# Performance work log

Hardware: AMD Instinct MI355X
Metric: run time of the kernel (lower is better)

Reference implementation:

```python
import jax, jax.numpy as jnp
import numpy as np
from jax import lax

B, S, K, H, NCLS = 64, 2048, 2, 256, 2
D = K * K  # input_dim = conv_kernel ** 2


def setup_inputs() -> dict:
    key = jax.random.key(0)
    ks = jax.random.split(key, 12)
    s = 0.1
    return {
        "x": jax.random.normal(ks[0], (B, S, D), dtype=jnp.float32),
        # elementwise quanvolution-style conv filter (k x k)
        "conv_w": jax.random.normal(ks[1], (K, K), dtype=jnp.float32) * s,
        "conv_b": jax.random.normal(ks[2], (K, K), dtype=jnp.float32) * s,
        # LSTM params, torch gate order (i, f, g, o)
        "w_ih": jax.random.normal(ks[3], (4 * H, D), dtype=jnp.float32) * s,
        "w_hh": jax.random.normal(ks[4], (4 * H, H), dtype=jnp.float32) * s,
        "b_ih": jax.random.normal(ks[5], (4 * H,), dtype=jnp.float32) * s,
        "b_hh": jax.random.normal(ks[6], (4 * H,), dtype=jnp.float32) * s,
        # classifier: depth=2 ReLU layers + final Linear(H, NCLS)
        "w1": jax.random.normal(ks[7], (H, H), dtype=jnp.float32) * s,
        "b1": jnp.zeros((H,), dtype=jnp.float32),
        "w2": jax.random.normal(ks[8], (H, H), dtype=jnp.float32) * s,
        "b2": jnp.zeros((H,), dtype=jnp.float32),
        "w3": jax.random.normal(ks[9], (NCLS, H), dtype=jnp.float32) * s,
        "b3": jnp.zeros((NCLS,), dtype=jnp.float32),
    }


def _lstm(feat, w_ih, w_hh, b_ih, b_hh):
    # feat: [B, S, D] -> hidden states [B, S, H]
    b, _, _ = feat.shape
    h_dim = w_hh.shape[1]
    bias = b_ih + b_hh
    # precompute input projections for all timesteps (batched GEMM)
    gates_x = jnp.einsum('bsd,gd->bsg', feat, w_ih) + bias  # [B, S, 4H]

    def step(carry, gx):
        h, c = carry
        gates = gx + h @ w_hh.T  # [B, 4H]
        i, f, g, o = jnp.split(gates, 4, axis=-1)
        i, f, o = jax.nn.sigmoid(i), jax.nn.sigmoid(f), jax.nn.sigmoid(o)
        g = jnp.tanh(g)
        c = f * c + i * g
        h = o * jnp.tanh(c)
        return (h, c), h

    init = (jnp.zeros((b, h_dim), feat.dtype), jnp.zeros((b, h_dim), feat.dtype))
    _, hs = lax.scan(step, init, gates_x.transpose(1, 0, 2))  # hs: [S, B, H]
    return hs.transpose(1, 0, 2)


def reference(x, conv_w, conv_b, w_ih, w_hh, b_ih, b_hh, w1, b1, w2, b2, w3, b3):
    b, s, _ = x.shape
    # batched replacement of the per-patch CPU conv loop
    patches = x.reshape(b, s, K, K)
    feat = jax.nn.sigmoid(patches * conv_w + conv_b).reshape(b, s, K * K)
    lstm_out = _lstm(feat, w_ih, w_hh, b_ih, b_hh)  # [B, S, H]
    h1 = jax.nn.relu(lstm_out @ w1.T + b1)
    h2 = jax.nn.relu(h1 @ w2.T + b2)
    logits = h2 @ w3.T + b3  # [B, S, NCLS]
    return logits
```

## Files before the change

kernel.cpp:

```cpp
#include <hip/hip_runtime.h>


#define BB 64
#define SS 2048
#define HH 256

typedef _Float16 f16;
typedef _Float16 h2 __attribute__((ext_vector_type(2)));
typedef _Float16 v8h __attribute__((ext_vector_type(8)));

union V8H { v8h v; h2 p[4]; };

__device__ __forceinline__ float fdot2f(h2 a, h2 b, float c){
#if __has_builtin(__builtin_amdgcn_fdot2)
  return __builtin_amdgcn_fdot2(a, b, c, false);
#else
  return c + (float)a.x*(float)b.x + (float)a.y*(float)b.y;
#endif
}

__device__ __forceinline__ float psum2(float x){
#if __has_builtin(__builtin_amdgcn_mov_dpp)
  x += __int_as_float(__builtin_amdgcn_mov_dpp(__float_as_int(x), 0xB1, 0xf, 0xf, true));
#else
  x += __shfl_xor(x, 1, 64);
#endif
  return x;
}

__device__ __forceinline__ float rcpf_(float x){
#if __has_builtin(__builtin_amdgcn_rcpf)
  return __builtin_amdgcn_rcpf(x);
#else
  return 1.f/x;
#endif
}
__device__ __forceinline__ float sigmf_(float x){ return rcpf_(1.f + __expf(-x)); }
__device__ __forceinline__ float tanhf_(float x){
  x = fminf(fmaxf(x, -15.f), 15.f);
  float e = __expf(2.f*x);
  return (e - 1.f)*rcpf_(e + 1.f);
}
__device__ __forceinline__ h2 mkh2(float a, float b){ h2 r; r.x=(f16)a; r.y=(f16)b; return r; }

__device__ __forceinline__ void lds_barrier(){
  asm volatile("s_waitcnt lgkmcnt(0)\n\ts_barrier" ::: "memory");
}

__global__ void prep_kernel(
    const float* __restrict__ x, const float* __restrict__ conv_w, const float* __restrict__ conv_b,
    const float* __restrict__ w_ih, const float* __restrict__ w_hh,
    const float* __restrict__ b_ih, const float* __restrict__ b_hh,
    const float* __restrict__ w1, const float* __restrict__ w2, const float* __restrict__ w3,
    f16* __restrict__ feat2, f16* __restrict__ wihp,
    float* __restrict__ biasp, f16* __restrict__ w1t, f16* __restrict__ w2t, f16* __restrict__ w3p)
{
  int id = blockIdx.x*256 + threadIdx.x;
  if (id < BB*SS){
    float4 xv = *(const float4*)(x + (size_t)id*4);
    float f0 = sigmf_(xv.x*conv_w[0] + conv_b[0]);
    float f1 = sigmf_(xv.y*conv_w[1] + conv_b[1]);
    float f2 = sigmf_(xv.z*conv_w[2] + conv_b[2]);
    float f3 = sigmf_(xv.w*conv_w[3] + conv_b[3]);
    h2* o = (h2*)feat2 + (size_t)id*2;
    o[0] = mkh2(f0,f1); o[1] = mkh2(f2,f3);
    return;
  }
  id -= BB*SS;
  if (id < 1024){
    int u = id >> 2;
    f16* o = wihp + (size_t)id*16;
    float bb[4];
    #pragma unroll
    for (int i=0;i<4;i++){
      int row = u + 256*i;
      o[i*4+0] = (f16)w_ih[row*4+0];
      o[i*4+1] = (f16)w_ih[row*4+1];
      o[i*4+2] = (f16)w_ih[row*4+2];
      o[i*4+3] = (f16)w_ih[row*4+3];
      bb[i] = b_ih[row] + b_hh[row];
    }
    *(float4*)(biasp + (size_t)id*4) = make_float4(bb[0],bb[1],bb[2],bb[3]);
    return;
  }
  id -= 1024;
  if (id < 32768){
    int kp = id >> 8, n = id & 255;
    w1t[(size_t)id*2+0] = (f16)w1[(size_t)n*256 + 2*kp];
    w1t[(size_t)id*2+1] = (f16)w1[(size_t)n*256 + 2*kp+1];
    return;
  }
  id -= 32768;
  if (id < 32768){
    int kp = id >> 8, n = id & 255;
    w2t[(size_t)id*2+0] = (f16)w2[(size_t)n*256 + 2*kp];
    w2t[(size_t)id*2+1] = (f16)w2[(size_t)n*256 + 2*kp+1];
    return;
  }
  id -= 32768;
  if (id < 256){
    int kp = id >> 1, cls = id & 1;
    w3p[(size_t)id*2+0] = (f16)w3[(size_t)cls*256 + 2*kp];
    w3p[(size_t)id*2+1] = (f16)w3[(size_t)cls*256 + 2*kp+1];
  }
}

#define GSEGV 17

__global__ __launch_bounds__(512, 2) void lstm_kernel(
    const float* __restrict__ w_hh, const f16* __restrict__ feat2,
    const f16* __restrict__ wihp, const float* __restrict__ biasp,
    f16* __restrict__ hbuf)
{
  extern __shared__ __align__(16) f16 glds[];
  const int b = blockIdx.x, t = threadIdx.x;
  const int u = t >> 1, hf = t & 1;
  __shared__ __align__(16) f16 hsh[2][2][136];

  h2 wi[64], wf[64], wo[64];
  {
    const float* si = w_hh + (size_t)u*256       + hf*128;
    const float* sf = w_hh + (size_t)(u+256)*256 + hf*128;
    const float* so = w_hh + (size_t)(u+768)*256 + hf*128;
    #pragma unroll
    for (int c=0;c<16;c++){
      float4 a = *(const float4*)(si + c*8);
      float4 q = *(const float4*)(si + c*8 + 4);
      wi[c*4+0] = mkh2(a.x,a.y); wi[c*4+1] = mkh2(a.z,a.w);
      wi[c*4+2] = mkh2(q.x,q.y); wi[c*4+3] = mkh2(q.z,q.w);
      a = *(const float4*)(sf + c*8);
      q = *(const float4*)(sf + c*8 + 4);
      wf[c*4+0] = mkh2(a.x,a.y); wf[c*4+1] = mkh2(a.z,a.w);
      wf[c*4+2] = mkh2(q.x,q.y); wf[c*4+3] = mkh2(q.z,q.w);
      a = *(const float4*)(so + c*8);
      q = *(const float4*)(so + c*8 + 4);
      wo[c*4+0] = mkh2(a.x,a.y); wo[c*4+1] = mkh2(a.z,a.w);
      wo[c*4+2] = mkh2(q.x,q.y); wo[c*4+3] = mkh2(q.z,q.w);
    }
  }
  {
    const float* sg = w_hh + (size_t)(512+u)*256 + hf*128;
    v8h* gdst = (v8h*)glds + (size_t)t*GSEGV;
    #pragma unroll
    for (int c=0;c<16;c++){
      float4 a = *(const float4*)(sg + c*8);
      float4 q = *(const float4*)(sg + c*8 + 4);
      v8h o;
      o[0]=(f16)a.x; o[1]=(f16)a.y; o[2]=(f16)a.z; o[3]=(f16)a.w;
      o[4]=(f16)q.x; o[5]=(f16)q.y; o[6]=(f16)q.z; o[7]=(f16)q.w;
      gdst[c] = o;
    }
  }
  h2 wx[8];
  {
    const h2* p = (const h2*)(wihp + (size_t)(t*2)*16);
    #pragma unroll
    for (int j=0;j<8;j++) wx[j] = p[j];
  }
  const float4 bsv = *(const float4*)(biasp + (size_t)(t*2)*4);

  if (t < 256) hsh[0][t>>7][t&127] = (f16)0.f;
  __syncthreads();

  const v8h* gp = (const v8h*)glds + (size_t)t*GSEGV;
  const h2* fp = (const h2*)feat2 + (size_t)b*SS*2;
  f16* hrow = hbuf + (size_t)b*SS*HH;
  const h2 ONE = mkh2(1.f, 1.f);
  const h2 ZERO = mkh2(0.f, 0.f);
  float cst = 0.f;
  int buf = 0;

  for (int s=0; s<SS; ++s){
    h2 f0 = fp[0], f1 = fp[1]; fp += 2;
    const v8h* hq = (const v8h*)(&hsh[buf][hf][0]);
    h2 accI[4], accF[4], accG[4], accO[4];
    #pragma unroll
    for (int k=0;k<4;k++){ accI[k]=ZERO; accF[k]=ZERO; accG[k]=ZERO; accO[k]=ZERO; }
    #pragma unroll
    for (int c=0;c<16;c++){
      V8H hv; hv.v = hq[c];
      V8H gv; gv.v = gp[c];
      #pragma unroll
      for (int k=0;k<4;k++){
        h2 p = hv.p[k];
        accI[k] = wi[c*4+k]*p + accI[k];
        accF[k] = wf[c*4+k]*p + accF[k];
        accG[k] = gv.p[k]  *p + accG[k];
        accO[k] = wo[c*4+k]*p + accO[k];
      }
    }
    float a0 = fdot2f(accI[3], ONE, fdot2f(accI[2], ONE, fdot2f(accI[1], ONE, fdot2f(accI[0], ONE, 0.f))));
    float a1 = fdot2f(accF[3], ONE, fdot2f(accF[2], ONE, fdot2f(accF[1], ONE, fdot2f(accF[0], ONE, 0.f))));
    float a2 = fdot2f(accG[3], ONE, fdot2f(accG[2], ONE, fdot2f(accG[1], ONE, fdot2f(accG[0], ONE, 0.f))));
    float a3 = fdot2f(accO[3], ONE, fdot2f(accO[2], ONE, fdot2f(accO[1], ONE, fdot2f(accO[0], ONE, 0.f))));
    a0 = psum2(a0); a1 = psum2(a1); a2 = psum2(a2); a3 = psum2(a3);
    float gi = fdot2f(wx[1], f1, fdot2f(wx[0], f0, a0 + bsv.x));
    float gf = fdot2f(wx[3], f1, fdot2f(wx[2], f0, a1 + bsv.y));
    float gg = fdot2f(wx[5], f1, fdot2f(wx[4], f0, a2 + bsv.z));
    float go = fdot2f(wx[7], f1, fdot2f(wx[6], f0, a3 + bsv.w));
    float iv = sigmf_(gi), fv = sigmf_(gf), gv2 = tanhf_(gg), ov = sigmf_(go);
    cst = fv*cst + iv*gv2;
    float hn = ov * tanhf_(cst);
    if (hf == 0){
      hsh[buf^1][u>>7][u&127] = (f16)hn;
    } else {
      hrow[u] = (f16)hn;
    }
    hrow += HH;
    lds_barrier();
    buf ^= 1;
  }
}

__device__ __forceinline__ void fc_layer(const h2 (*src)[20], h2 (*dst)[20],
                                         const f16* __restrict__ wt,
                                         const float* __restrict__ bias, int t)
{
  const int rg = t >> 6;
  const int c0 = (t & 63) * 4;
  float acc[4][4];
  #pragma unroll
  for (int r=0;r<4;r++){ acc[r][0]=0.f; acc[r][1]=0.f; acc[r][2]=0.f; acc[r][3]=0.f; }
  #pragma unroll 4
  for (int kp=0; kp<128; kp++){
    V8H wv; wv.v = *(const v8h*)(wt + ((size_t)kp*256 + c0)*2);
    V8H rv; rv.v = *(const v8h*)(&src[kp][rg*4]);
    #pragma unroll
    for (int r=0;r<4;r++)
      #pragma unroll
      for (int c=0;c<4;c++)
        acc[r][c] = fdot2f(rv.p[r], wv.p[c], acc[r][c]);
  }
  const float4 bv = *(const float4*)(bias + c0);
  #pragma unroll
  for (int r=0;r<4;r++){
    float o0 = fmaxf(acc[r][0]+bv.x, 0.f);
    float o1 = fmaxf(acc[r][1]+bv.y, 0.f);
    float o2 = fmaxf(acc[r][2]+bv.z, 0.f);
    float o3 = fmaxf(acc[r][3]+bv.w, 0.f);
    dst[(c0>>1)  ][rg*4+r] = mkh2(o0,o1);
    dst[(c0>>1)+1][rg*4+r] = mkh2(o2,o3);
  }
}

__global__ __launch_bounds__(256) void cls_kernel(
    const f16* __restrict__ hbuf, const f16* __restrict__ w1t, const f16* __restrict__ w2t,
    const f16* __restrict__ w3p, const float* __restrict__ b1, const float* __restrict__ b2,
    const float* __restrict__ b3, float* __restrict__ out)
{
  __shared__ __align__(16) h2 rlA[128][20];
  __shared__ __align__(16) h2 rlB[128][20];
  const int t = threadIdx.x;
  const size_t R = (size_t)blockIdx.x * 16;
  {
    int r = t >> 4, seg = t & 15;
    const v8h* src = (const v8h*)(hbuf + (R + r)*HH + seg*16);
    V8H aH; aH.v = src[0];
    V8H bH; bH.v = src[1];
    int kp0 = seg*8;
    #pragma unroll
    for (int j=0;j<4;j++) rlA[kp0+j  ][r] = aH.p[j];
    #pragma unroll
    for (int j=0;j<4;j++) rlA[kp0+4+j][r] = bH.p[j];
  }
  __syncthreads();
  fc_layer(rlA, rlB, w1t, b1, t);
  __syncthreads();
  fc_layer(rlB, rlA, w2t, b2, t);
  __syncthreads();
  if (t < 32){
    int r = t >> 1, cls = t & 1;
    float acc = b3[cls];
    const h2* w3h = (const h2*)w3p;
    #pragma unroll 8
    for (int kp=0; kp<128; kp++)
      acc = fdot2f(rlA[kp][r], w3h[kp*2 + cls], acc);
    out[(R + r)*2 + cls] = acc;
  }
}

extern "C" void kernel_launch(void* const* d_in, const int* in_sizes, int n_in,
                              void* d_out, int out_size, void* d_ws, size_t ws_size,
                              hipStream_t stream) {
  const float* x      = (const float*)d_in[0];
  const float* conv_w = (const float*)d_in[1];
  const float* conv_b = (const float*)d_in[2];
  const float* w_ih   = (const float*)d_in[3];
  const float* w_hh   = (const float*)d_in[4];
  const float* b_ih   = (const float*)d_in[5];
  const float* b_hh   = (const float*)d_in[6];
  const float* w1     = (const float*)d_in[7];
  const float* b1     = (const float*)d_in[8];
  const float* w2     = (const float*)d_in[9];
  const float* b2     = (const float*)d_in[10];
  const float* w3     = (const float*)d_in[11];
  const float* b3     = (const float*)d_in[12];

  char* ws = (char*)d_ws;
  f16*   feat2   = (f16*)  (ws + 0x000000);
  f16*   wihp    = (f16*)  (ws + 0x100000);
  float* biasp   = (float*)(ws + 0x108000);
  f16*   w1t     = (f16*)  (ws + 0x10C000);
  f16*   w2t     = (f16*)  (ws + 0x12C000);
  f16*   w3p     = (f16*)  (ws + 0x14C000);
  f16*   hbuf    = (f16*)  (ws + 0x150000);

  const int glds_bytes = 512 * GSEGV * 16;
  (void)hipFuncSetAttribute((const void*)lstm_kernel,
                            hipFuncAttributeMaxDynamicSharedMemorySize, glds_bytes);

  prep_kernel<<<773, 256, 0, stream>>>(x, conv_w, conv_b, w_ih, w_hh, b_ih, b_hh,
                                       w1, w2, w3,
                                       feat2, wihp, biasp, w1t, w2t, w3p);
  lstm_kernel<<<BB, 512, glds_bytes, stream>>>(w_hh, feat2, wihp, biasp, hbuf);
  cls_kernel<<<(BB*SS)/16, 256, 0, stream>>>(hbuf, w1t, w2t, w3p, b1, b2, b3, (float*)d_out);
}
```

Measured before the change: 3.597 ms.

## Use MFMA for LSTM recurrent matvec with prepacked W_hh fragments

```diff
diff --git a/kernel.cpp b/kernel.cpp
--- a/kernel.cpp
+++ b/kernel.cpp
@@ -8,6 +8,7 @@
 typedef _Float16 f16;
 typedef _Float16 h2 __attribute__((ext_vector_type(2)));
 typedef _Float16 v8h __attribute__((ext_vector_type(8)));
+typedef float f32x4 __attribute__((ext_vector_type(4)));
 
 union V8H { v8h v; h2 p[4]; };
 
@@ -19,15 +20,6 @@
 #endif
 }
 
-__device__ __forceinline__ float psum2(float x){
-#if __has_builtin(__builtin_amdgcn_mov_dpp)
-  x += __int_as_float(__builtin_amdgcn_mov_dpp(__float_as_int(x), 0xB1, 0xf, 0xf, true));
-#else
-  x += __shfl_xor(x, 1, 64);
-#endif
-  return x;
-}
-
 __device__ __forceinline__ float rcpf_(float x){
 #if __has_builtin(__builtin_amdgcn_rcpf)
   return __builtin_amdgcn_rcpf(x);
@@ -52,8 +44,8 @@
     const float* __restrict__ w_ih, const float* __restrict__ w_hh,
     const float* __restrict__ b_ih, const float* __restrict__ b_hh,
     const float* __restrict__ w1, const float* __restrict__ w2, const float* __restrict__ w3,
-    f16* __restrict__ feat2, f16* __restrict__ wihp,
-    float* __restrict__ biasp, f16* __restrict__ w1t, f16* __restrict__ w2t, f16* __restrict__ w3p)
+    f16* __restrict__ feat2, f16* __restrict__ Bpack, f16* __restrict__ wihb,
+    f16* __restrict__ w1t, f16* __restrict__ w2t, f16* __restrict__ w3p)
 {
   int id = blockIdx.x*256 + threadIdx.x;
   if (id < BB*SS){
@@ -67,23 +59,34 @@
     return;
   }
   id -= BB*SS;
-  if (id < 1024){
-    int u = id >> 2;
-    f16* o = wihp + (size_t)id*16;
-    float bb[4];
-    #pragma unroll
-    for (int i=0;i<4;i++){
-      int row = u + 256*i;
-      o[i*4+0] = (f16)w_ih[row*4+0];
-      o[i*4+1] = (f16)w_ih[row*4+1];
-      o[i*4+2] = (f16)w_ih[row*4+2];
-      o[i*4+3] = (f16)w_ih[row*4+3];
-      bb[i] = b_ih[row] + b_hh[row];
+  if (id < 32768){
+    int l = id & 63, k = (id>>6)&7, t = (id>>9)&15, w = (id>>13)&3;
+    int n  = (t>>2)*256 + w*64 + (t&3)*16 + (l&15);
+    int kk = k*32 + (l>>4)*8;
+    const float* src = w_hh + (size_t)n*256 + kk;
+    v8h o;
+    #pragma unroll
+    for (int j=0;j<8;j++) o[j] = (f16)src[j];
+    *((v8h*)Bpack + id) = o;
+    return;
+  }
+  id -= 32768;
+  if (id < 64){
+    int w = id >> 4, c = id & 15;
+    f16* e = wihb + (size_t)id*96;
+    float* bf = (float*)(e + 64);
+    #pragma unroll
+    for (int t=0;t<16;t++){
+      int n = (t>>2)*256 + w*64 + (t&3)*16 + c;
+      e[t*4+0] = (f16)w_ih[n*4+0];
+      e[t*4+1] = (f16)w_ih[n*4+1];
+      e[t*4+2] = (f16)w_ih[n*4+2];
+      e[t*4+3] = (f16)w_ih[n*4+3];
+      bf[t] = b_ih[n] + b_hh[n];
     }
-    *(float4*)(biasp + (size_t)id*4) = make_float4(bb[0],bb[1],bb[2],bb[3]);
-    return;
-  }
-  id -= 1024;
+    return;
+  }
+  id -= 64;
   if (id < 32768){
     int kp = id >> 8, n = id & 255;
     w1t[(size_t)id*2+0] = (f16)w1[(size_t)n*256 + 2*kp];
@@ -105,106 +108,103 @@
   }
 }
 
-#define GSEGV 17
-
-__global__ __launch_bounds__(512, 2) void lstm_kernel(
-    const float* __restrict__ w_hh, const f16* __restrict__ feat2,
-    const f16* __restrict__ wihp, const float* __restrict__ biasp,
-    f16* __restrict__ hbuf)
+#define LDS_H    131072
+#define LDS_WIHB 132096
+#define GLDS_BYTES 144384
+
+__global__ __launch_bounds__(256, 1) void lstm_kernel(
+    const f16* __restrict__ Bpack, const f16* __restrict__ feat2,
+    const f16* __restrict__ wihb, f16* __restrict__ hbuf)
 {
-  extern __shared__ __align__(16) f16 glds[];
-  const int b = blockIdx.x, t = threadIdx.x;
-  const int u = t >> 1, hf = t & 1;
-  __shared__ __align__(16) f16 hsh[2][2][136];
-
-  h2 wi[64], wf[64], wo[64];
+  extern __shared__ __align__(16) char glds[];
+  const int b = blockIdx.x, tid = threadIdx.x;
+  const int w = tid >> 6, l = tid & 63;
+  const int grp = l >> 4, c = l & 15;
+
+  const v8h* bp = (const v8h*)Bpack + (size_t)w*16*8*64;
+  v8h breg[12][8];
+  #pragma unroll
+  for (int t=0;t<12;t++)
+    #pragma unroll
+    for (int k=0;k<8;k++)
+      breg[t][k] = bp[(t*8+k)*64 + l];
+
   {
-    const float* si = w_hh + (size_t)u*256       + hf*128;
-    const float* sf = w_hh + (size_t)(u+256)*256 + hf*128;
-    const float* so = w_hh + (size_t)(u+768)*256 + hf*128;
-    #pragma unroll
-    for (int c=0;c<16;c++){
-      float4 a = *(const float4*)(si + c*8);
-      float4 q = *(const float4*)(si + c*8 + 4);
-      wi[c*4+0] = mkh2(a.x,a.y); wi[c*4+1] = mkh2(a.z,a.w);
-      wi[c*4+2] = mkh2(q.x,q.y); wi[c*4+3] = mkh2(q.z,q.w);
-      a = *(const float4*)(sf + c*8);
-      q = *(const float4*)(sf + c*8 + 4);
-      wf[c*4+0] = mkh2(a.x,a.y); wf[c*4+1] = mkh2(a.z,a.w);
-      wf[c*4+2] = mkh2(q.x,q.y); wf[c*4+3] = mkh2(q.z,q.w);
-      a = *(const float4*)(so + c*8);
-      q = *(const float4*)(so + c*8 + 4);
-      wo[c*4+0] = mkh2(a.x,a.y); wo[c*4+1] = mkh2(a.z,a.w);
-      wo[c*4+2] = mkh2(q.x,q.y); wo[c*4+3] = mkh2(q.z,q.w);
-    }
+    f16* bl = (f16*)glds + (size_t)w*16384;
+    #pragma unroll
+    for (int t2=0;t2<4;t2++)
+      #pragma unroll
+      for (int k=0;k<8;k++){
+        v8h v = bp[((12+t2)*8+k)*64 + l];
+        *(v8h*)(bl + (t2*8+k)*512 + l*8) = v;
+      }
   }
   {
-    const float* sg = w_hh + (size_t)(512+u)*256 + hf*128;
-    v8h* gdst = (v8h*)glds + (size_t)t*GSEGV;
-    #pragma unroll
-    for (int c=0;c<16;c++){
-      float4 a = *(const float4*)(sg + c*8);
-      float4 q = *(const float4*)(sg + c*8 + 4);
-      v8h o;
-      o[0]=(f16)a.x; o[1]=(f16)a.y; o[2]=(f16)a.z; o[3]=(f16)a.w;
-      o[4]=(f16)q.x; o[5]=(f16)q.y; o[6]=(f16)q.z; o[7]=(f16)q.w;
-      gdst[c] = o;
-    }
-  }
-  h2 wx[8];
-  {
-    const h2* p = (const h2*)(wihp + (size_t)(t*2)*16);
-    #pragma unroll
-    for (int j=0;j<8;j++) wx[j] = p[j];
-  }
-  const float4 bsv = *(const float4*)(biasp + (size_t)(t*2)*4);
-
-  if (t < 256) hsh[0][t>>7][t&127] = (f16)0.f;
+    const int* src = (const int*)wihb;
+    int* dst = (int*)(glds + LDS_WIHB);
+    for (int i = tid; i < 3072; i += 256) dst[i] = src[i];
+  }
+  f16* hb = (f16*)(glds + LDS_H);
+  if (tid < 256){ hb[tid] = (f16)0.f; hb[256+tid] = (f16)0.f; }
   __syncthreads();
 
-  const v8h* gp = (const v8h*)glds + (size_t)t*GSEGV;
   const h2* fp = (const h2*)feat2 + (size_t)b*SS*2;
   f16* hrow = hbuf + (size_t)b*SS*HH;
-  const h2 ONE = mkh2(1.f, 1.f);
-  const h2 ZERO = mkh2(0.f, 0.f);
-  float cst = 0.f;
+  const f16* wl  = (const f16*)(glds + LDS_WIHB) + (size_t)(w*16 + c)*96;
+  const float* blf = (const float*)(wl + 64);
+  const f16* bldsr = (const f16*)glds + (size_t)w*16384 + l*8;
+  float cst[4] = {0.f,0.f,0.f,0.f};
   int buf = 0;
+  const f32x4 Z4 = {0.f,0.f,0.f,0.f};
 
   for (int s=0; s<SS; ++s){
     h2 f0 = fp[0], f1 = fp[1]; fp += 2;
-    const v8h* hq = (const v8h*)(&hsh[buf][hf][0]);
-    h2 accI[4], accF[4], accG[4], accO[4];
-    #pragma unroll
-    for (int k=0;k<4;k++){ accI[k]=ZERO; accF[k]=ZERO; accG[k]=ZERO; accO[k]=ZERO; }
-    #pragma unroll
-    for (int c=0;c<16;c++){
-      V8H hv; hv.v = hq[c];
-      V8H gv; gv.v = gp[c];
+    const f16* hq = hb + buf*256 + grp*8;
+    f32x4 acc[16];
+    #pragma unroll
+    for (int k=0;k<8;k++){
+      v8h a = *(const v8h*)(hq + k*32);
       #pragma unroll
-      for (int k=0;k<4;k++){
-        h2 p = hv.p[k];
-        accI[k] = wi[c*4+k]*p + accI[k];
-        accF[k] = wf[c*4+k]*p + accF[k];
-        accG[k] = gv.p[k]  *p + accG[k];
-        accO[k] = wo[c*4+k]*p + accO[k];
+      for (int t=0;t<12;t++){
+        f32x4 cin = (k==0) ? Z4 : acc[t];
+        acc[t] = __builtin_amdgcn_mfma_f32_16x16x32_f16(a, breg[t][k], cin, 0,0,0);
+      }
+      #pragma unroll
+      for (int t2=0;t2<4;t2++){
+        v8h bv = *(const v8h*)(bldsr + (t2*8+k)*512);
+        f32x4 cin = (k==0) ? Z4 : acc[12+t2];
+        acc[12+t2] = __builtin_amdgcn_mfma_f32_16x16x32_f16(a, bv, cin, 0,0,0);
       }
     }
-    float a0 = fdot2f(accI[3], ONE, fdot2f(accI[2], ONE, fdot2f(accI[1], ONE, fdot2f(accI[0], ONE, 0.f))));
-    float a1 = fdot2f(accF[3], ONE, fdot2f(accF[2], ONE, fdot2f(accF[1], ONE, fdot2f(accF[0], ONE, 0.f))));
-    float a2 = fdot2f(accG[3], ONE, fdot2f(accG[2], ONE, fdot2f(accG[1], ONE, fdot2f(accG[0], ONE, 0.f))));
-    float a3 = fdot2f(accO[3], ONE, fdot2f(accO[2], ONE, fdot2f(accO[1], ONE, fdot2f(accO[0], ONE, 0.f))));
-    a0 = psum2(a0); a1 = psum2(a1); a2 = psum2(a2); a3 = psum2(a3);
-    float gi = fdot2f(wx[1], f1, fdot2f(wx[0], f0, a0 + bsv.x));
-    float gf = fdot2f(wx[3], f1, fdot2f(wx[2], f0, a1 + bsv.y));
-    float gg = fdot2f(wx[5], f1, fdot2f(wx[4], f0, a2 + bsv.z));
-    float go = fdot2f(wx[7], f1, fdot2f(wx[6], f0, a3 + bsv.w));
-    float iv = sigmf_(gi), fv = sigmf_(gf), gv2 = tanhf_(gg), ov = sigmf_(go);
-    cst = fv*cst + iv*gv2;
-    float hn = ov * tanhf_(cst);
-    if (hf == 0){
-      hsh[buf^1][u>>7][u&127] = (f16)hn;
-    } else {
-      hrow[u] = (f16)hn;
+    float pre[16];
+    #pragma unroll
+    for (int t=0;t<16;t++) pre[t] = acc[t][0];
+    V8H wv[8];
+    #pragma unroll
+    for (int i=0;i<8;i++) wv[i].v = *(const v8h*)(wl + i*8);
+    f32x4 bq[4];
+    #pragma unroll
+    for (int q=0;q<4;q++) bq[q] = *(const f32x4*)(blf + q*4);
+    #pragma unroll
+    for (int t=0;t<16;t++){
+      h2 wa = wv[t>>1].p[(t&1)*2];
+      h2 wb = wv[t>>1].p[(t&1)*2+1];
+      pre[t] = fdot2f(wb, f1, fdot2f(wa, f0, pre[t] + bq[t>>2][t&3]));
+    }
+    #pragma unroll
+    for (int a2=0;a2<4;a2++){
+      float iv = sigmf_(pre[a2]);
+      float fv = sigmf_(pre[4+a2]);
+      float gv = tanhf_(pre[8+a2]);
+      float ov = sigmf_(pre[12+a2]);
+      cst[a2] = fv*cst[a2] + iv*gv;
+      float hn = ov*tanhf_(cst[a2]);
+      if (l < 16){
+        int u = w*64 + a2*16 + c;
+        f16 hv = (f16)hn;
+        hb[(buf^1)*256 + u] = hv;
+        hrow[u] = hv;
+      }
     }
     hrow += HH;
     lds_barrier();
@@ -228,8 +228,8 @@
     #pragma unroll
     for (int r=0;r<4;r++)
       #pragma unroll
-      for (int c=0;c<4;c++)
-        acc[r][c] = fdot2f(rv.p[r], wv.p[c], acc[r][c]);
+      for (int cc=0;cc<4;cc++)
+        acc[r][cc] = fdot2f(rv.p[r], wv.p[cc], acc[r][cc]);
   }
   const float4 bv = *(const float4*)(bias + c0);
   #pragma unroll
@@ -298,20 +298,19 @@
 
   char* ws = (char*)d_ws;
   f16*   feat2   = (f16*)  (ws + 0x000000);
-  f16*   wihp    = (f16*)  (ws + 0x100000);
-  float* biasp   = (float*)(ws + 0x108000);
-  f16*   w1t     = (f16*)  (ws + 0x10C000);
-  f16*   w2t     = (f16*)  (ws + 0x12C000);
-  f16*   w3p     = (f16*)  (ws + 0x14C000);
-  f16*   hbuf    = (f16*)  (ws + 0x150000);
-
-  const int glds_bytes = 512 * GSEGV * 16;
+  f16*   Bpack   = (f16*)  (ws + 0x100000);
+  f16*   wihb    = (f16*)  (ws + 0x180000);
+  f16*   w1t     = (f16*)  (ws + 0x190000);
+  f16*   w2t     = (f16*)  (ws + 0x1B0000);
+  f16*   w3p     = (f16*)  (ws + 0x1D0000);
+  f16*   hbuf    = (f16*)  (ws + 0x1E0000);
+
   (void)hipFuncSetAttribute((const void*)lstm_kernel,
-                            hipFuncAttributeMaxDynamicSharedMemorySize, glds_bytes);
-
-  prep_kernel<<<773, 256, 0, stream>>>(x, conv_w, conv_b, w_ih, w_hh, b_ih, b_hh,
+                            hipFuncAttributeMaxDynamicSharedMemorySize, GLDS_BYTES);
+
+  prep_kernel<<<898, 256, 0, stream>>>(x, conv_w, conv_b, w_ih, w_hh, b_ih, b_hh,
                                        w1, w2, w3,
-                                       feat2, wihp, biasp, w1t, w2t, w3p);
-  lstm_kernel<<<BB, 512, glds_bytes, stream>>>(w_hh, feat2, wihp, biasp, hbuf);
+                                       feat2, Bpack, wihb, w1t, w2t, w3p);
+  lstm_kernel<<<BB, 256, GLDS_BYTES, stream>>>(Bpack, feat2, wihb, hbuf);
   cls_kernel<<<(BB*SS)/16, 256, 0, stream>>>(hbuf, w1t, w2t, w3p, b1, b2, b3, (float*)d_out);
 }
```

Measured after the change: 5.796 ms. +61.1%, slower.
